# Kernel optimization log

Measured on AMD Instinct MI355X. Metric: run time of the kernel, lower is better.

The kernel has to match this reference:

```python
import jax, jax.numpy as jnp
import numpy as np

CN = 1024   # concept_num
H = 64      # hidden_dim
E = 64      # embedding_dim
RES_LEN = 2 # binary=True
B = 256     # batch (students)
D = H + E   # mlp_input_dim


def _mlp(x, W1, b1, W2, b2):
    # GKT MLP: relu(fc1) -> dropout(eval: identity) -> relu(fc2)
    return jax.nn.relu(jax.nn.relu(x @ W1 + b1) @ W2 + b2)


def setup_inputs() -> dict:
    key = jax.random.key(0)
    ks = jax.random.split(key, 20)
    s = 0.05
    nrm = lambda k, shape, scale=s: jax.random.normal(k, shape, dtype=jnp.float32) * scale
    zeros = lambda shape: jnp.zeros(shape, jnp.float32)
    return {
        "xt": jax.random.randint(ks[0], (B,), 0, RES_LEN * CN),
        "qt": jax.random.randint(ks[1], (B,), 0, CN),
        "ht": nrm(ks[2], (B, CN, H), 1.0),
        "graph": jax.random.uniform(ks[3], (CN, CN), dtype=jnp.float32),
        "emb_x": nrm(ks[4], (RES_LEN * CN, E), 1.0),
        "emb_c": nrm(ks[5], (CN + 1, E), 1.0).at[CN].set(0.0),  # padding row
        "fs_W1": nrm(ks[6], (D, H)), "fs_b1": zeros((H,)),
        "fs_W2": nrm(ks[7], (H, H)), "fs_b2": zeros((H,)),
        "fn0_W1": nrm(ks[8], (2 * D, H)), "fn0_b1": zeros((H,)),
        "fn0_W2": nrm(ks[9], (H, H)), "fn0_b2": zeros((H,)),
        "fn1_W1": nrm(ks[10], (2 * D, H)), "fn1_b1": zeros((H,)),
        "fn1_W2": nrm(ks[11], (H, H)), "fn1_b2": zeros((H,)),
        "ea_weight": jax.random.uniform(ks[12], (CN,), dtype=jnp.float32),
        "erase_W": nrm(ks[13], (H, H)), "erase_b": zeros((H,)),
        "add_W": nrm(ks[14], (H, H)), "add_b": zeros((H,)),
        "gru_Wih": nrm(ks[15], (H, 3 * H)), "gru_bih": zeros((3 * H,)),
        "gru_Whh": nrm(ks[16], (H, 3 * H)), "gru_bhh": zeros((3 * H,)),
        "pred_W": nrm(ks[17], (H, 1)), "pred_b": zeros((1,)),
    }


def _forward(xt, qt, graph, ht, emb_x, emb_c,
             fs_W1, fs_b1, fs_W2, fs_b2,
             fn0_W1, fn0_b1, fn0_W2, fn0_b2,
             fn1_W1, fn1_b1, fn1_W2, fn1_b2,
             ea_weight, erase_W, erase_b, add_W, add_b,
             gru_Wih, gru_bih, gru_Whh, gru_bhh, pred_W, pred_b):
    qt_mask = qt != -1                                   # [B]
    qts = jnp.clip(qt, 0, CN - 1)
    # ---------- _aggregate ----------
    res_emb = emb_x[xt]                                  # [B,E] == onehot(xt) @ emb_x
    base = jnp.where(qt_mask[:, None, None], emb_c[None, :CN, :], emb_c[CN][None, None, :])
    at_q = (jnp.arange(CN)[None, :] == qts[:, None]) & qt_mask[:, None]  # [B,CN]
    concept_emb = jnp.where(at_q[..., None], res_emb[:, None, :], base)  # [B,CN,E]
    tmp_ht = jnp.concatenate([ht, concept_emb], axis=-1)  # [B,CN,D]
    # ---------- _adj ----------
    adj = graph[qts][..., None]                          # [B,CN,1]
    radj = graph[:, qts].T[..., None]                    # [B,CN,1]
    # ---------- _agg_neighbors ----------
    self_ht = tmp_ht[jnp.arange(B), qts]                 # [B,D]
    self_feat = _mlp(self_ht, fs_W1, fs_b1, fs_W2, fs_b2)  # [B,H]
    neigh_ht = jnp.concatenate(
        [jnp.broadcast_to(self_ht[:, None, :], (B, CN, D)), tmp_ht], axis=-1)  # [B,CN,2D]
    neigh_feat = adj * _mlp(neigh_ht, fn0_W1, fn0_b1, fn0_W2, fn0_b2) \
               + radj * _mlp(neigh_ht, fn1_W1, fn1_b1, fn1_W2, fn1_b2)  # [B,CN,H]
    m_next = jnp.where(qt_mask[:, None, None], neigh_feat, ht)
    m_next = jnp.where(at_q[..., None], self_feat[:, None, :], m_next)
    # ---------- erase-add gate on masked rows ----------
    erase_g = jax.nn.sigmoid(m_next @ erase_W + erase_b)
    add_f = jnp.tanh(m_next @ add_W + add_b)
    w = ea_weight[None, :, None]                         # per-concept gate weight
    gated = m_next - w * erase_g * m_next + w * add_f
    m_next = jnp.where(qt_mask[:, None, None], gated, m_next)
    # ---------- GRUCell update on masked rows ----------
    gi = m_next @ gru_Wih + gru_bih                      # [B,CN,3H]
    gh = ht @ gru_Whh + gru_bhh
    i_r, i_z, i_n = jnp.split(gi, 3, axis=-1)
    h_r, h_z, h_n = jnp.split(gh, 3, axis=-1)
    r = jax.nn.sigmoid(i_r + h_r)
    z = jax.nn.sigmoid(i_z + h_z)
    n = jnp.tanh(i_n + r * h_n)
    h_gru = (1.0 - z) * n + z * ht
    h_next = jnp.where(qt_mask[:, None, None], h_gru, m_next)
    # ---------- _predict ----------
    y = (h_next @ pred_W + pred_b)[..., 0]               # [B,CN]
    y = jnp.where(qt_mask[:, None], jax.nn.sigmoid(y), y)
    return y


def reference(xt, qt, ht, graph, emb_x, emb_c,
              fs_W1, fs_b1, fs_W2, fs_b2,
              fn0_W1, fn0_b1, fn0_W2, fn0_b2,
              fn1_W1, fn1_b1, fn1_W2, fn1_b2,
              ea_weight, erase_W, erase_b, add_W, add_b,
              gru_Wih, gru_bih, gru_Whh, gru_bhh, pred_W, pred_b):
    return _forward(xt, qt, graph, ht, emb_x, emb_c,
                    fs_W1, fs_b1, fs_W2, fs_b2,
                    fn0_W1, fn0_b1, fn0_W2, fn0_b2,
                    fn1_W1, fn1_b1, fn1_W2, fn1_b2,
                    ea_weight, erase_W, erase_b, add_W, add_b,
                    gru_Wih, gru_bih, gru_Whh, gru_bhh, pred_W, pred_b)
```

## Files before the change

kernel.cpp:

```cpp
#include <hip/hip_runtime.h>
#include <hip/hip_bf16.h>

#define CN 1024
#define BN 256
#define SMEM_BYTES 155392

typedef __attribute__((ext_vector_type(4))) float f32x4;
typedef __attribute__((ext_vector_type(8))) short bf16x8;

__device__ __forceinline__ short f2bf(float f) {
    __hip_bfloat16 h = __float2bfloat16(f);
    return *reinterpret_cast<short*>(&h);
}
__device__ __forceinline__ float sigm(float x) {
    return __builtin_amdgcn_rcpf(1.f + __expf(-x));
}
__device__ __forceinline__ float tanh_fast(float x) {
    return 1.f - 2.f * __builtin_amdgcn_rcpf(1.f + __expf(2.f * x));
}

__global__ __launch_bounds__(256) void gkt_prep(
    const int* __restrict__ xt, const int* __restrict__ qt,
    const float* __restrict__ ht, const float* __restrict__ emb_x,
    const float* __restrict__ emb_c,
    const float* __restrict__ fs_W1, const float* __restrict__ fs_b1,
    const float* __restrict__ fs_W2, const float* __restrict__ fs_b2,
    const float* __restrict__ fn0_W1, const float* __restrict__ fn0_b1,
    const float* __restrict__ fn0_W2, const float* __restrict__ fn0_b2,
    const float* __restrict__ fn1_W1, const float* __restrict__ fn1_b1,
    const float* __restrict__ fn1_W2, const float* __restrict__ fn1_b2,
    const float* __restrict__ erase_W, const float* __restrict__ erase_b,
    const float* __restrict__ add_W, const float* __restrict__ add_b,
    const float* __restrict__ gru_Wih, const float* __restrict__ gru_bih,
    const float* __restrict__ gru_Whh, const float* __restrict__ gru_bhh,
    short* __restrict__ wrepack, float* __restrict__ biasc,
    float* __restrict__ perb, int* __restrict__ qtsA,
    int* __restrict__ maskA, int* __restrict__ xeA)
{
    int bid = blockIdx.x;
    int tid = threadIdx.x;
    int lane = tid & 63, wv = tid >> 6;
    __shared__ float inp[4][128];
    __shared__ float t1s[4][64];

    if (bid < 14) {
        int t = bid * 4 + wv;
        int colg = t * 16 + (lane & 15);
#pragma unroll
        for (int kh = 0; kh < 2; ++kh) {
            int k0 = kh * 32 + (lane >> 4) * 8;
            short v8[8];
#pragma unroll
            for (int j = 0; j < 8; ++j) {
                int k = k0 + j;
                float v;
                if (colg < 64)       v = fn0_W1[(128 + k) * 64 + colg];
                else if (colg < 128) v = fn1_W1[(128 + k) * 64 + (colg - 64)];
                else if (colg < 320) v = gru_Whh[k * 192 + (colg - 128)];
                else if (colg < 384) v = fn0_W2[k * 64 + (colg - 320)];
                else if (colg < 448) v = fn1_W2[k * 64 + (colg - 384)];
                else if (colg < 512) v = erase_W[k * 64 + (colg - 448)];
                else if (colg < 576) v = add_W[k * 64 + (colg - 512)];
                else if (colg < 768) v = gru_Wih[k * 192 + (colg - 576)];
                else if (colg < 832) v = fn0_W1[(192 + k) * 64 + (colg - 768)];
                else                 v = fn1_W1[(192 + k) * 64 + (colg - 832)];
                v8[j] = f2bf(v);
            }
            short* dst = wrepack + ((size_t)(t * 2 + kh) * 64 + lane) * 8;
#pragma unroll
            for (int j = 0; j < 8; ++j) dst[j] = v8[j];
        }
    } else if (bid == 14) {
        for (int g = tid; g < 768; g += 256) {
            float v;
            if (g < 64)       v = fn0_b1[g];
            else if (g < 128) v = fn1_b1[g - 64];
            else if (g < 320) v = gru_bhh[g - 128];
            else if (g < 384) v = fn0_b2[g - 320];
            else if (g < 448) v = fn1_b2[g - 384];
            else if (g < 512) v = erase_b[g - 448];
            else if (g < 576) v = add_b[g - 512];
            else              v = gru_bih[g - 576];
            biasc[g] = v;
        }
    } else {
        int b = (bid - 15) * 4 + wv;
        int qv = qt[b];
        int mki = (qv != -1);
        int qs = min(max(qv, 0), CN - 1);
        int xe = xt[b];
        float cq = mki ? emb_x[(size_t)xe * 64 + lane]
                       : emb_c[(size_t)CN * 64 + lane];
        inp[wv][lane]      = ht[((size_t)b * CN + qs) * 64 + lane];
        inp[wv][64 + lane] = cq;
        float p0 = 0.f, p1 = 0.f, fs = 0.f;
        for (int k = 0; k < 128; ++k) {
            float xk = inp[wv][k];
            p0 += xk * fn0_W1[k * 64 + lane];
            p1 += xk * fn1_W1[k * 64 + lane];
            fs += xk * fs_W1[k * 64 + lane];
        }
        t1s[wv][lane] = fmaxf(fs + fs_b1[lane], 0.f);
        float sf = 0.f;
        for (int k = 0; k < 64; ++k) sf += t1s[wv][k] * fs_W2[k * 64 + lane];
        sf = fmaxf(sf + fs_b2[lane], 0.f);
        float* pd = perb + (size_t)b * 192;
        pd[lane] = p0; pd[64 + lane] = p1; pd[128 + lane] = sf;
        if (lane == 0) { qtsA[b] = qs; maskA[b] = mki; xeA[b] = xe; }
    }
}

#define MFMA(a, bf, c) __builtin_amdgcn_mfma_f32_16x16x32_bf16((a), (bf), (c), 0, 0, 0)

__global__ __launch_bounds__(512, 1) void gkt_main(
    const float* __restrict__ ht, const float* __restrict__ graph,
    const float* __restrict__ ea_w, const float* __restrict__ pred_W,
    const float* __restrict__ pred_b,
    const short* __restrict__ wrepack, const float* __restrict__ biasc,
    const float* __restrict__ perb, const int* __restrict__ qtsA,
    const int* __restrict__ maskA, const int* __restrict__ xeA,
    const float* __restrict__ emb_x, const float* __restrict__ emb_c,
    float* __restrict__ out)
{
    extern __shared__ char smem[];
    short* FRs    = (short*)smem;
    float* s_bias = (float*)(smem + 114688);
    float* s_pre  = (float*)(smem + 117760);
    short* tiles  = (short*)(smem + 118528);

    int tid = threadIdx.x;
    int lane = tid & 63, w = tid >> 6;
    int l15 = lane & 15, q = lane >> 4;
    int b = blockIdx.x;

    short* s_x0 = tiles + w * 2304;
    short* s_x1 = s_x0 + 1152;

    {
        const f32x4* src = (const f32x4*)wrepack;
        f32x4* dst = (f32x4*)FRs;
        for (int i = tid; i < 7168; i += 512) dst[i] = src[i];
        for (int i = tid; i < 768; i += 512) s_bias[i] = biasc[i];
        const float* pd = perb + (size_t)b * 192;
        if (tid < 192) s_pre[tid] = pd[tid];
    }
    int qts = qtsA[b];
    int mk  = maskA[b];
    int xe  = xeA[b];
    __syncthreads();

    const bf16x8* FR = (const bf16x8*)FRs;
    f32x4 zero4 = {0.f, 0.f, 0.f, 0.f};
    float pb0 = pred_b[0];
    float pw[4];
#pragma unroll
    for (int t = 0; t < 4; ++t) pw[t] = pred_W[t * 16 + l15];

    for (int rt = 0; rt < 8; ++rt) {
        int c0 = w * 128 + rt * 16;
        const float* hrow = ht + ((size_t)b * CN + c0 + l15) * 64;
        f32x4 a0 = *(const f32x4*)(hrow + 8 * q);
        f32x4 a1 = *(const f32x4*)(hrow + 8 * q + 4);
        f32x4 a2 = *(const f32x4*)(hrow + 8 * q + 32);
        f32x4 a3 = *(const f32x4*)(hrow + 8 * q + 36);

        if (!mk) {
            f32x4 pwa = *(const f32x4*)(pred_W + 8 * q);
            f32x4 pwb = *(const f32x4*)(pred_W + 8 * q + 4);
            f32x4 pwc = *(const f32x4*)(pred_W + 8 * q + 32);
            f32x4 pwd = *(const f32x4*)(pred_W + 8 * q + 36);
            float part = 0.f;
#pragma unroll
            for (int i = 0; i < 4; ++i)
                part += a0[i] * pwa[i] + a1[i] * pwb[i] + a2[i] * pwc[i] + a3[i] * pwd[i];
            part += __shfl_xor(part, 16);
            part += __shfl_xor(part, 32);
            if (q == 0) out[(size_t)b * CN + c0 + l15] = part + pb0;
            continue;
        }

        int rq = c0 + l15;
        const float* ep = (rq == qts) ? (emb_x + (size_t)xe * 64)
                                      : (emb_c + (size_t)rq * 64);
        f32x4 e0 = *(const f32x4*)(ep + 8 * q);
        f32x4 e1 = *(const f32x4*)(ep + 8 * q + 4);
        f32x4 e2 = *(const f32x4*)(ep + 8 * q + 32);
        f32x4 e3 = *(const f32x4*)(ep + 8 * q + 36);

        bf16x8 hA0, hA1, cA0, cA1;
#pragma unroll
        for (int j = 0; j < 4; ++j) {
            hA0[j] = f2bf(a0[j]); hA0[4 + j] = f2bf(a1[j]);
            hA1[j] = f2bf(a2[j]); hA1[4 + j] = f2bf(a3[j]);
            cA0[j] = f2bf(e0[j]); cA0[4 + j] = f2bf(e1[j]);
            cA1[j] = f2bf(e2[j]); cA1[4 + j] = f2bf(e3[j]);
        }

        float adjv[4], radjv[4], eav[4];
#pragma unroll
        for (int r = 0; r < 4; ++r) {
            int cr = c0 + q * 4 + r;
            adjv[r]  = graph[(size_t)qts * CN + cr];
            radjv[r] = graph[(size_t)cr * CN + qts];
            eav[r]   = ea_w[cr];
        }
        float hv[4][4];
#pragma unroll
        for (int t = 0; t < 4; ++t)
#pragma unroll
            for (int r = 0; r < 4; ++r)
                hv[t][r] = ht[((size_t)b * CN + c0 + q * 4 + r) * 64 + t * 16 + l15];

#pragma unroll
        for (int t = 0; t < 8; ++t) {
            f32x4 acc = MFMA(hA0, FR[(2 * t) * 64 + lane], zero4);
            acc = MFMA(hA1, FR[(2 * t + 1) * 64 + lane], acc);
            acc = MFMA(cA0, FR[(96 + 2 * t) * 64 + lane], acc);
            acc = MFMA(cA1, FR[(97 + 2 * t) * 64 + lane], acc);
            int jl = (t & 3) * 16 + l15;
            float base = s_bias[t * 16 + l15] + ((t < 4) ? s_pre[jl] : s_pre[64 + jl]);
#pragma unroll
            for (int r = 0; r < 4; ++r) {
                float u = fmaxf(acc[r] + base, 0.f);
                if (t < 4) s_x0[(q * 4 + r) * 72 + jl] = f2bf(u);
                else       s_x1[(q * 4 + r) * 72 + jl] = f2bf(u);
            }
        }

        bf16x8 x0A0 = *(const bf16x8*)(s_x0 + l15 * 72 + 8 * q);
        bf16x8 x0A1 = *(const bf16x8*)(s_x0 + l15 * 72 + 32 + 8 * q);
        bf16x8 x1A0 = *(const bf16x8*)(s_x1 + l15 * 72 + 8 * q);
        bf16x8 x1A1 = *(const bf16x8*)(s_x1 + l15 * 72 + 32 + 8 * q);
        float mreg[4][4];
#pragma unroll
        for (int t = 0; t < 4; ++t) {
            f32x4 f0a = MFMA(x0A0, FR[(40 + 2 * t) * 64 + lane], zero4);
            f0a = MFMA(x0A1, FR[(41 + 2 * t) * 64 + lane], f0a);
            f32x4 f1a = MFMA(x1A0, FR[(48 + 2 * t) * 64 + lane], zero4);
            f1a = MFMA(x1A1, FR[(49 + 2 * t) * 64 + lane], f1a);
            int jl = t * 16 + l15;
            float b0 = s_bias[320 + jl], b1 = s_bias[384 + jl];
#pragma unroll
            for (int r = 0; r < 4; ++r) {
                int cr = c0 + q * 4 + r;
                float f0 = fmaxf(f0a[r] + b0, 0.f), f1 = fmaxf(f1a[r] + b1, 0.f);
                float mv = adjv[r] * f0 + radjv[r] * f1;
                if (cr == qts) mv = s_pre[128 + jl];
                mreg[t][r] = mv;
            }
        }
#pragma unroll
        for (int t = 0; t < 4; ++t)
#pragma unroll
            for (int r = 0; r < 4; ++r)
                s_x0[(q * 4 + r) * 72 + t * 16 + l15] = f2bf(mreg[t][r]);

        bf16x8 mA0 = *(const bf16x8*)(s_x0 + l15 * 72 + 8 * q);
        bf16x8 mA1 = *(const bf16x8*)(s_x0 + l15 * 72 + 32 + 8 * q);
#pragma unroll
        for (int t = 0; t < 4; ++t) {
            f32x4 eacc = MFMA(mA0, FR[(56 + 2 * t) * 64 + lane], zero4);
            eacc = MFMA(mA1, FR[(57 + 2 * t) * 64 + lane], eacc);
            f32x4 aacc = MFMA(mA0, FR[(64 + 2 * t) * 64 + lane], zero4);
            aacc = MFMA(mA1, FR[(65 + 2 * t) * 64 + lane], aacc);
            int jl = t * 16 + l15;
            float be = s_bias[448 + jl], ba = s_bias[512 + jl];
#pragma unroll
            for (int r = 0; r < 4; ++r) {
                float eg = sigm(eacc[r] + be);
                float af = tanh_fast(aacc[r] + ba);
                float mp = mreg[t][r] * (1.f - eav[r] * eg) + eav[r] * af;
                s_x1[(q * 4 + r) * 72 + jl] = f2bf(mp);
            }
        }

        bf16x8 mpA0 = *(const bf16x8*)(s_x1 + l15 * 72 + 8 * q);
        bf16x8 mpA1 = *(const bf16x8*)(s_x1 + l15 * 72 + 32 + 8 * q);
        float rg[4][4], ng[4][4];
#pragma unroll
        for (int t = 0; t < 4; ++t) {
            f32x4 gi = MFMA(mpA0, FR[(72 + 2 * t) * 64 + lane], zero4);
            gi = MFMA(mpA1, FR[(73 + 2 * t) * 64 + lane], gi);
            f32x4 gh = MFMA(hA0, FR[(16 + 2 * t) * 64 + lane], zero4);
            gh = MFMA(hA1, FR[(17 + 2 * t) * 64 + lane], gh);
            int jl = t * 16 + l15;
            float bi = s_bias[576 + jl], bh = s_bias[128 + jl];
#pragma unroll
            for (int r = 0; r < 4; ++r)
                rg[t][r] = sigm(gi[r] + bi + gh[r] + bh);
        }
#pragma unroll
        for (int t = 0; t < 4; ++t) {
            f32x4 gi = MFMA(mpA0, FR[(88 + 2 * t) * 64 + lane], zero4);
            gi = MFMA(mpA1, FR[(89 + 2 * t) * 64 + lane], gi);
            f32x4 gh = MFMA(hA0, FR[(32 + 2 * t) * 64 + lane], zero4);
            gh = MFMA(hA1, FR[(33 + 2 * t) * 64 + lane], gh);
            int jl = t * 16 + l15;
            float bi = s_bias[704 + jl], bh = s_bias[256 + jl];
#pragma unroll
            for (int r = 0; r < 4; ++r)
                ng[t][r] = tanh_fast(gi[r] + bi + rg[t][r] * (gh[r] + bh));
        }
        float yp[4] = {0.f, 0.f, 0.f, 0.f};
#pragma unroll
        for (int t = 0; t < 4; ++t) {
            f32x4 gi = MFMA(mpA0, FR[(80 + 2 * t) * 64 + lane], zero4);
            gi = MFMA(mpA1, FR[(81 + 2 * t) * 64 + lane], gi);
            f32x4 gh = MFMA(hA0, FR[(24 + 2 * t) * 64 + lane], zero4);
            gh = MFMA(hA1, FR[(25 + 2 * t) * 64 + lane], gh);
            int jl = t * 16 + l15;
            float bi = s_bias[640 + jl], bh = s_bias[192 + jl];
#pragma unroll
            for (int r = 0; r < 4; ++r) {
                float z = sigm(gi[r] + bi + gh[r] + bh);
                float hn = (1.f - z) * ng[t][r] + z * hv[t][r];
                yp[r] += hn * pw[t];
            }
        }
#pragma unroll
        for (int r = 0; r < 4; ++r) {
            float v = yp[r];
            v += __shfl_xor(v, 1);
            v += __shfl_xor(v, 2);
            v += __shfl_xor(v, 4);
            v += __shfl_xor(v, 8);
            if (l15 == 0) out[(size_t)b * CN + c0 + q * 4 + r] = sigm(v + pb0);
        }
    }
}

extern "C" void kernel_launch(void* const* d_in, const int* in_sizes, int n_in,
                              void* d_out, int out_size, void* d_ws, size_t ws_size,
                              hipStream_t stream) {
    (void)in_sizes; (void)n_in; (void)out_size; (void)ws_size;
    const int*   xt      = (const int*)d_in[0];
    const int*   qt      = (const int*)d_in[1];
    const float* ht      = (const float*)d_in[2];
    const float* graph   = (const float*)d_in[3];
    const float* emb_x   = (const float*)d_in[4];
    const float* emb_c   = (const float*)d_in[5];
    const float* fs_W1   = (const float*)d_in[6];
    const float* fs_b1   = (const float*)d_in[7];
    const float* fs_W2   = (const float*)d_in[8];
    const float* fs_b2   = (const float*)d_in[9];
    const float* fn0_W1  = (const float*)d_in[10];
    const float* fn0_b1  = (const float*)d_in[11];
    const float* fn0_W2  = (const float*)d_in[12];
    const float* fn0_b2  = (const float*)d_in[13];
    const float* fn1_W1  = (const float*)d_in[14];
    const float* fn1_b1  = (const float*)d_in[15];
    const float* fn1_W2  = (const float*)d_in[16];
    const float* fn1_b2  = (const float*)d_in[17];
    const float* ea_w    = (const float*)d_in[18];
    const float* erase_W = (const float*)d_in[19];
    const float* erase_b = (const float*)d_in[20];
    const float* add_W   = (const float*)d_in[21];
    const float* add_b   = (const float*)d_in[22];
    const float* gru_Wih = (const float*)d_in[23];
    const float* gru_bih = (const float*)d_in[24];
    const float* gru_Whh = (const float*)d_in[25];
    const float* gru_bhh = (const float*)d_in[26];
    const float* pred_W  = (const float*)d_in[27];
    const float* pred_b  = (const float*)d_in[28];

    char* ws = (char*)d_ws;
    short* wrepack = (short*)(ws);
    float* biasc   = (float*)(ws + 114688);
    float* perb    = (float*)(ws + 117760);
    int*   qtsA    = (int*)(ws + 314368);
    int*   maskA   = (int*)(ws + 315392);
    int*   xeA     = (int*)(ws + 316416);

    (void)hipFuncSetAttribute((const void*)gkt_main,
                              hipFuncAttributeMaxDynamicSharedMemorySize,
                              SMEM_BYTES);

    gkt_prep<<<79, 256, 0, stream>>>(
        xt, qt, ht, emb_x, emb_c,
        fs_W1, fs_b1, fs_W2, fs_b2,
        fn0_W1, fn0_b1, fn0_W2, fn0_b2,
        fn1_W1, fn1_b1, fn1_W2, fn1_b2,
        erase_W, erase_b, add_W, add_b,
        gru_Wih, gru_bih, gru_Whh, gru_bhh,
        wrepack, biasc, perb, qtsA, maskA, xeA);

    gkt_main<<<BN, 512, SMEM_BYTES, stream>>>(
        ht, graph, ea_w, pred_W, pred_b,
        wrepack, biasc, perb, qtsA, maskA, xeA,
        emb_x, emb_c, (float*)d_out);
}
```

Baseline: 219.8 us.

## Swap MFMA operand roles to keep activations in registers and drop LDS tiles

The MFMA operands are swapped so weights are the A operand and per-concept activations are the B operand, letting each layer's output feed the next layer straight from registers instead of round-tripping through per-wave LDS tiles. The weight repack permutes K order to match the register layout, and the r/z GRU biases are pre-summed. Block size doubles to 1024 threads with half the row tiles per wave, and LDS use shrinks. The risks are higher register pressure at 1024 threads and per-row scalar graph loads.

```diff
diff --git a/kernel.cpp b/kernel.cpp
--- a/kernel.cpp
+++ b/kernel.cpp
@@ -3,7 +3,7 @@
 
 #define CN 1024
 #define BN 256
-#define SMEM_BYTES 155392
+#define SMEM_BYTES 118016
 
 typedef __attribute__((ext_vector_type(4))) float f32x4;
 typedef __attribute__((ext_vector_type(8))) short bf16x8;
@@ -18,6 +18,7 @@
 __device__ __forceinline__ float tanh_fast(float x) {
     return 1.f - 2.f * __builtin_amdgcn_rcpf(1.f + __expf(2.f * x));
 }
+
 
 __global__ __launch_bounds__(256) void gkt_prep(
     const int* __restrict__ xt, const int* __restrict__ qt,
@@ -40,19 +41,19 @@
     int bid = blockIdx.x;
     int tid = threadIdx.x;
     int lane = tid & 63, wv = tid >> 6;
+    int l15 = lane & 15, q = lane >> 4;
     __shared__ float inp[4][128];
     __shared__ float t1s[4][64];
 
     if (bid < 14) {
         int t = bid * 4 + wv;
-        int colg = t * 16 + (lane & 15);
+        int colg = t * 16 + l15;
 #pragma unroll
         for (int kh = 0; kh < 2; ++kh) {
-            int k0 = kh * 32 + (lane >> 4) * 8;
             short v8[8];
 #pragma unroll
-            for (int j = 0; j < 8; ++j) {
-                int k = k0 + j;
+            for (int i = 0; i < 8; ++i) {
+                int k = kh * 32 + ((i >> 2) << 4) + (q << 2) + (i & 3);
                 float v;
                 if (colg < 64)       v = fn0_W1[(128 + k) * 64 + colg];
                 else if (colg < 128) v = fn1_W1[(128 + k) * 64 + (colg - 64)];
@@ -64,23 +65,25 @@
                 else if (colg < 768) v = gru_Wih[k * 192 + (colg - 576)];
                 else if (colg < 832) v = fn0_W1[(192 + k) * 64 + (colg - 768)];
                 else                 v = fn1_W1[(192 + k) * 64 + (colg - 832)];
-                v8[j] = f2bf(v);
+                v8[i] = f2bf(v);
             }
             short* dst = wrepack + ((size_t)(t * 2 + kh) * 64 + lane) * 8;
 #pragma unroll
-            for (int j = 0; j < 8; ++j) dst[j] = v8[j];
+            for (int i = 0; i < 8; ++i) dst[i] = v8[i];
         }
     } else if (bid == 14) {
-        for (int g = tid; g < 768; g += 256) {
+        for (int g = tid; g < 640; g += 256) {
             float v;
             if (g < 64)       v = fn0_b1[g];
             else if (g < 128) v = fn1_b1[g - 64];
-            else if (g < 320) v = gru_bhh[g - 128];
+            else if (g < 192) v = gru_bih[g - 128] + gru_bhh[g - 128];
+            else if (g < 256) v = gru_bih[g - 128] + gru_bhh[g - 128];
+            else if (g < 320) v = gru_bih[128 + (g - 256)];
             else if (g < 384) v = fn0_b2[g - 320];
             else if (g < 448) v = fn1_b2[g - 384];
             else if (g < 512) v = erase_b[g - 448];
             else if (g < 576) v = add_b[g - 512];
-            else              v = gru_bih[g - 576];
+            else              v = gru_bhh[128 + (g - 576)];
             biasc[g] = v;
         }
     } else {
@@ -110,9 +113,9 @@
     }
 }
 
-#define MFMA(a, bf, c) __builtin_amdgcn_mfma_f32_16x16x32_bf16((a), (bf), (c), 0, 0, 0)
-
-__global__ __launch_bounds__(512, 1) void gkt_main(
+#define MFMA(wa, xb, c) __builtin_amdgcn_mfma_f32_16x16x32_bf16((wa), (xb), (c), 0, 0, 0)
+
+__global__ __launch_bounds__(1024, 1) void gkt_main(
     const float* __restrict__ ht, const float* __restrict__ graph,
     const float* __restrict__ ea_w, const float* __restrict__ pred_W,
     const float* __restrict__ pred_b,
@@ -125,24 +128,20 @@
     extern __shared__ char smem[];
     short* FRs    = (short*)smem;
     float* s_bias = (float*)(smem + 114688);
-    float* s_pre  = (float*)(smem + 117760);
-    short* tiles  = (short*)(smem + 118528);
+    float* s_pre  = (float*)(smem + 117248);
 
     int tid = threadIdx.x;
     int lane = tid & 63, w = tid >> 6;
     int l15 = lane & 15, q = lane >> 4;
     int b = blockIdx.x;
 
-    short* s_x0 = tiles + w * 2304;
-    short* s_x1 = s_x0 + 1152;
-
     {
         const f32x4* src = (const f32x4*)wrepack;
         f32x4* dst = (f32x4*)FRs;
-        for (int i = tid; i < 7168; i += 512) dst[i] = src[i];
-        for (int i = tid; i < 768; i += 512) s_bias[i] = biasc[i];
+        for (int i = tid; i < 7168; i += 1024) dst[i] = src[i];
+        if (tid < 640) s_bias[tid] = biasc[tid];
         const float* pd = perb + (size_t)b * 192;
-        if (tid < 192) s_pre[tid] = pd[tid];
+        if (tid >= 640 && tid < 832) s_pre[tid - 640] = pd[tid - 640];
     }
     int qts = qtsA[b];
     int mk  = maskA[b];
@@ -152,180 +151,164 @@
     const bf16x8* FR = (const bf16x8*)FRs;
     f32x4 zero4 = {0.f, 0.f, 0.f, 0.f};
     float pb0 = pred_b[0];
-    float pw[4];
-#pragma unroll
-    for (int t = 0; t < 4; ++t) pw[t] = pred_W[t * 16 + l15];
-
-    for (int rt = 0; rt < 8; ++rt) {
-        int c0 = w * 128 + rt * 16;
-        const float* hrow = ht + ((size_t)b * CN + c0 + l15) * 64;
-        f32x4 a0 = *(const f32x4*)(hrow + 8 * q);
-        f32x4 a1 = *(const f32x4*)(hrow + 8 * q + 4);
-        f32x4 a2 = *(const f32x4*)(hrow + 8 * q + 32);
-        f32x4 a3 = *(const f32x4*)(hrow + 8 * q + 36);
+    f32x4 pw0 = *(const f32x4*)(pred_W + 4 * q);
+    f32x4 pw1 = *(const f32x4*)(pred_W + 16 + 4 * q);
+    f32x4 pw2 = *(const f32x4*)(pred_W + 32 + 4 * q);
+    f32x4 pw3 = *(const f32x4*)(pred_W + 48 + 4 * q);
+
+    for (int rt = 0; rt < 4; ++rt) {
+        int c0 = w * 64 + rt * 16;
+        int cr = c0 + l15;
+        const float* hrow = ht + ((size_t)b * CN + cr) * 64 + 4 * q;
+        f32x4 v0 = *(const f32x4*)(hrow);
+        f32x4 v1 = *(const f32x4*)(hrow + 16);
+        f32x4 v2 = *(const f32x4*)(hrow + 32);
+        f32x4 v3 = *(const f32x4*)(hrow + 48);
 
         if (!mk) {
-            f32x4 pwa = *(const f32x4*)(pred_W + 8 * q);
-            f32x4 pwb = *(const f32x4*)(pred_W + 8 * q + 4);
-            f32x4 pwc = *(const f32x4*)(pred_W + 8 * q + 32);
-            f32x4 pwd = *(const f32x4*)(pred_W + 8 * q + 36);
-            float part = 0.f;
+            float yp = 0.f;
 #pragma unroll
             for (int i = 0; i < 4; ++i)
-                part += a0[i] * pwa[i] + a1[i] * pwb[i] + a2[i] * pwc[i] + a3[i] * pwd[i];
-            part += __shfl_xor(part, 16);
-            part += __shfl_xor(part, 32);
-            if (q == 0) out[(size_t)b * CN + c0 + l15] = part + pb0;
+                yp += v0[i] * pw0[i] + v1[i] * pw1[i] + v2[i] * pw2[i] + v3[i] * pw3[i];
+            yp += __shfl_xor(yp, 16);
+            yp += __shfl_xor(yp, 32);
+            if (q == 0) out[(size_t)b * CN + cr] = yp + pb0;
             continue;
         }
 
-        int rq = c0 + l15;
-        const float* ep = (rq == qts) ? (emb_x + (size_t)xe * 64)
-                                      : (emb_c + (size_t)rq * 64);
-        f32x4 e0 = *(const f32x4*)(ep + 8 * q);
-        f32x4 e1 = *(const f32x4*)(ep + 8 * q + 4);
-        f32x4 e2 = *(const f32x4*)(ep + 8 * q + 32);
-        f32x4 e3 = *(const f32x4*)(ep + 8 * q + 36);
-
-        bf16x8 hA0, hA1, cA0, cA1;
-#pragma unroll
-        for (int j = 0; j < 4; ++j) {
-            hA0[j] = f2bf(a0[j]); hA0[4 + j] = f2bf(a1[j]);
-            hA1[j] = f2bf(a2[j]); hA1[4 + j] = f2bf(a3[j]);
-            cA0[j] = f2bf(e0[j]); cA0[4 + j] = f2bf(e1[j]);
-            cA1[j] = f2bf(e2[j]); cA1[4 + j] = f2bf(e3[j]);
-        }
-
-        float adjv[4], radjv[4], eav[4];
-#pragma unroll
-        for (int r = 0; r < 4; ++r) {
-            int cr = c0 + q * 4 + r;
-            adjv[r]  = graph[(size_t)qts * CN + cr];
-            radjv[r] = graph[(size_t)cr * CN + qts];
-            eav[r]   = ea_w[cr];
-        }
-        float hv[4][4];
-#pragma unroll
-        for (int t = 0; t < 4; ++t)
+        bool isq = (cr == qts);
+        const float* ep = isq ? (emb_x + (size_t)xe * 64)
+                              : (emb_c + (size_t)cr * 64);
+        f32x4 e0 = *(const f32x4*)(ep + 4 * q);
+        f32x4 e1 = *(const f32x4*)(ep + 16 + 4 * q);
+        f32x4 e2 = *(const f32x4*)(ep + 32 + 4 * q);
+        f32x4 e3 = *(const f32x4*)(ep + 48 + 4 * q);
+
+        bf16x8 hB0, hB1, cB0, cB1;
+#pragma unroll
+        for (int i = 0; i < 4; ++i) {
+            hB0[i] = f2bf(v0[i]); hB0[4 + i] = f2bf(v1[i]);
+            hB1[i] = f2bf(v2[i]); hB1[4 + i] = f2bf(v3[i]);
+            cB0[i] = f2bf(e0[i]); cB0[4 + i] = f2bf(e1[i]);
+            cB1[i] = f2bf(e2[i]); cB1[4 + i] = f2bf(e3[i]);
+        }
+
+        float adjs  = graph[(size_t)qts * CN + cr];
+        float radjs = graph[(size_t)cr * CN + qts];
+        float eas   = ea_w[cr];
+
+        bf16x8 x0B0, x0B1, x1B0, x1B1;
+#pragma unroll
+        for (int t = 0; t < 8; ++t) {
+            f32x4 acc = MFMA(FR[(2 * t) * 64 + lane], hB0, zero4);
+            acc = MFMA(FR[(2 * t + 1) * 64 + lane], hB1, acc);
+            acc = MFMA(FR[(96 + 2 * t) * 64 + lane], cB0, acc);
+            acc = MFMA(FR[(97 + 2 * t) * 64 + lane], cB1, acc);
+            int jb = (t & 3) * 16 + 4 * q;
+            f32x4 prev = *(const f32x4*)(s_pre + ((t < 4) ? 0 : 64) + jb);
+            f32x4 bv   = *(const f32x4*)(s_bias + t * 16 + 4 * q);
+#pragma unroll
+            for (int r = 0; r < 4; ++r) {
+                short us = f2bf(fmaxf(acc[r] + prev[r] + bv[r], 0.f));
+                if      (t == 0) x0B0[r] = us;
+                else if (t == 1) x0B0[4 + r] = us;
+                else if (t == 2) x0B1[r] = us;
+                else if (t == 3) x0B1[4 + r] = us;
+                else if (t == 4) x1B0[r] = us;
+                else if (t == 5) x1B0[4 + r] = us;
+                else if (t == 6) x1B1[r] = us;
+                else             x1B1[4 + r] = us;
+            }
+        }
+
+        f32x4 mreg0, mreg1, mreg2, mreg3;
+        bf16x8 mB0, mB1;
+#pragma unroll
+        for (int t = 0; t < 4; ++t) {
+            f32x4 f0a = MFMA(FR[(40 + 2 * t) * 64 + lane], x0B0, zero4);
+            f0a = MFMA(FR[(41 + 2 * t) * 64 + lane], x0B1, f0a);
+            f32x4 f1a = MFMA(FR[(48 + 2 * t) * 64 + lane], x1B0, zero4);
+            f1a = MFMA(FR[(49 + 2 * t) * 64 + lane], x1B1, f1a);
+            int jb = t * 16 + 4 * q;
+            f32x4 b0v = *(const f32x4*)(s_bias + 320 + jb);
+            f32x4 b1v = *(const f32x4*)(s_bias + 384 + jb);
+            f32x4 sfv = *(const f32x4*)(s_pre + 128 + jb);
+#pragma unroll
+            for (int r = 0; r < 4; ++r) {
+                float f0 = fmaxf(f0a[r] + b0v[r], 0.f);
+                float f1 = fmaxf(f1a[r] + b1v[r], 0.f);
+                float mv = adjs * f0 + radjs * f1;
+                mv = isq ? sfv[r] : mv;
+                if      (t == 0) { mreg0[r] = mv; mB0[r] = f2bf(mv); }
+                else if (t == 1) { mreg1[r] = mv; mB0[4 + r] = f2bf(mv); }
+                else if (t == 2) { mreg2[r] = mv; mB1[r] = f2bf(mv); }
+                else             { mreg3[r] = mv; mB1[4 + r] = f2bf(mv); }
+            }
+        }
+
+        bf16x8 pB0, pB1;
+#pragma unroll
+        for (int t = 0; t < 4; ++t) {
+            f32x4 eacc = MFMA(FR[(56 + 2 * t) * 64 + lane], mB0, zero4);
+            eacc = MFMA(FR[(57 + 2 * t) * 64 + lane], mB1, eacc);
+            f32x4 aacc = MFMA(FR[(64 + 2 * t) * 64 + lane], mB0, zero4);
+            aacc = MFMA(FR[(65 + 2 * t) * 64 + lane], mB1, aacc);
+            int jb = t * 16 + 4 * q;
+            f32x4 bev = *(const f32x4*)(s_bias + 448 + jb);
+            f32x4 bav = *(const f32x4*)(s_bias + 512 + jb);
+#pragma unroll
+            for (int r = 0; r < 4; ++r) {
+                float eg = sigm(eacc[r] + bev[r]);
+                float af = tanh_fast(aacc[r] + bav[r]);
+                float mr = (t == 0) ? mreg0[r] : (t == 1) ? mreg1[r]
+                         : (t == 2) ? mreg2[r] : mreg3[r];
+                float mp = mr * (1.f - eas * eg) + eas * af;
+                if      (t == 0) pB0[r] = f2bf(mp);
+                else if (t == 1) pB0[4 + r] = f2bf(mp);
+                else if (t == 2) pB1[r] = f2bf(mp);
+                else             pB1[4 + r] = f2bf(mp);
+            }
+        }
+
+        float yp = 0.f;
+#pragma unroll
+        for (int t = 0; t < 4; ++t) {
+            int jb = t * 16 + 4 * q;
+            f32x4 gir = MFMA(FR[(72 + 2 * t) * 64 + lane], pB0, zero4);
+            gir = MFMA(FR[(73 + 2 * t) * 64 + lane], pB1, gir);
+            f32x4 ghr = MFMA(FR[(16 + 2 * t) * 64 + lane], hB0, zero4);
+            ghr = MFMA(FR[(17 + 2 * t) * 64 + lane], hB1, ghr);
+            f32x4 brv = *(const f32x4*)(s_bias + 128 + jb);
+            f32x4 rg;
+#pragma unroll
+            for (int r = 0; r < 4; ++r) rg[r] = sigm(gir[r] + ghr[r] + brv[r]);
+            f32x4 gin = MFMA(FR[(88 + 2 * t) * 64 + lane], pB0, zero4);
+            gin = MFMA(FR[(89 + 2 * t) * 64 + lane], pB1, gin);
+            f32x4 ghn = MFMA(FR[(32 + 2 * t) * 64 + lane], hB0, zero4);
+            ghn = MFMA(FR[(33 + 2 * t) * 64 + lane], hB1, ghn);
+            f32x4 binv = *(const f32x4*)(s_bias + 256 + jb);
+            f32x4 bhnv = *(const f32x4*)(s_bias + 576 + jb);
+            f32x4 ng;
 #pragma unroll
             for (int r = 0; r < 4; ++r)
-                hv[t][r] = ht[((size_t)b * CN + c0 + q * 4 + r) * 64 + t * 16 + l15];
-
-#pragma unroll
-        for (int t = 0; t < 8; ++t) {
-            f32x4 acc = MFMA(hA0, FR[(2 * t) * 64 + lane], zero4);
-            acc = MFMA(hA1, FR[(2 * t + 1) * 64 + lane], acc);
-            acc = MFMA(cA0, FR[(96 + 2 * t) * 64 + lane], acc);
-            acc = MFMA(cA1, FR[(97 + 2 * t) * 64 + lane], acc);
-            int jl = (t & 3) * 16 + l15;
-            float base = s_bias[t * 16 + l15] + ((t < 4) ? s_pre[jl] : s_pre[64 + jl]);
+                ng[r] = tanh_fast(gin[r] + binv[r] + rg[r] * (ghn[r] + bhnv[r]));
+            f32x4 giz = MFMA(FR[(80 + 2 * t) * 64 + lane], pB0, zero4);
+            giz = MFMA(FR[(81 + 2 * t) * 64 + lane], pB1, giz);
+            f32x4 ghz = MFMA(FR[(24 + 2 * t) * 64 + lane], hB0, zero4);
+            ghz = MFMA(FR[(25 + 2 * t) * 64 + lane], hB1, ghz);
+            f32x4 bzv = *(const f32x4*)(s_bias + 192 + jb);
+            f32x4 hvv = (t == 0) ? v0 : (t == 1) ? v1 : (t == 2) ? v2 : v3;
+            f32x4 pwv = (t == 0) ? pw0 : (t == 1) ? pw1 : (t == 2) ? pw2 : pw3;
 #pragma unroll
             for (int r = 0; r < 4; ++r) {
-                float u = fmaxf(acc[r] + base, 0.f);
-                if (t < 4) s_x0[(q * 4 + r) * 72 + jl] = f2bf(u);
-                else       s_x1[(q * 4 + r) * 72 + jl] = f2bf(u);
-            }
-        }
-
-        bf16x8 x0A0 = *(const bf16x8*)(s_x0 + l15 * 72 + 8 * q);
-        bf16x8 x0A1 = *(const bf16x8*)(s_x0 + l15 * 72 + 32 + 8 * q);
-        bf16x8 x1A0 = *(const bf16x8*)(s_x1 + l15 * 72 + 8 * q);
-        bf16x8 x1A1 = *(const bf16x8*)(s_x1 + l15 * 72 + 32 + 8 * q);
-        float mreg[4][4];
-#pragma unroll
-        for (int t = 0; t < 4; ++t) {
-            f32x4 f0a = MFMA(x0A0, FR[(40 + 2 * t) * 64 + lane], zero4);
-            f0a = MFMA(x0A1, FR[(41 + 2 * t) * 64 + lane], f0a);
-            f32x4 f1a = MFMA(x1A0, FR[(48 + 2 * t) * 64 + lane], zero4);
-            f1a = MFMA(x1A1, FR[(49 + 2 * t) * 64 + lane], f1a);
-            int jl = t * 16 + l15;
-            float b0 = s_bias[320 + jl], b1 = s_bias[384 + jl];
-#pragma unroll
-            for (int r = 0; r < 4; ++r) {
-                int cr = c0 + q * 4 + r;
-                float f0 = fmaxf(f0a[r] + b0, 0.f), f1 = fmaxf(f1a[r] + b1, 0.f);
-                float mv = adjv[r] * f0 + radjv[r] * f1;
-                if (cr == qts) mv = s_pre[128 + jl];
-                mreg[t][r] = mv;
-            }
-        }
-#pragma unroll
-        for (int t = 0; t < 4; ++t)
-#pragma unroll
-            for (int r = 0; r < 4; ++r)
-                s_x0[(q * 4 + r) * 72 + t * 16 + l15] = f2bf(mreg[t][r]);
-
-        bf16x8 mA0 = *(const bf16x8*)(s_x0 + l15 * 72 + 8 * q);
-        bf16x8 mA1 = *(const bf16x8*)(s_x0 + l15 * 72 + 32 + 8 * q);
-#pragma unroll
-        for (int t = 0; t < 4; ++t) {
-            f32x4 eacc = MFMA(mA0, FR[(56 + 2 * t) * 64 + lane], zero4);
-            eacc = MFMA(mA1, FR[(57 + 2 * t) * 64 + lane], eacc);
-            f32x4 aacc = MFMA(mA0, FR[(64 + 2 * t) * 64 + lane], zero4);
-            aacc = MFMA(mA1, FR[(65 + 2 * t) * 64 + lane], aacc);
-            int jl = t * 16 + l15;
-            float be = s_bias[448 + jl], ba = s_bias[512 + jl];
-#pragma unroll
-            for (int r = 0; r < 4; ++r) {
-                float eg = sigm(eacc[r] + be);
-                float af = tanh_fast(aacc[r] + ba);
-                float mp = mreg[t][r] * (1.f - eav[r] * eg) + eav[r] * af;
-                s_x1[(q * 4 + r) * 72 + jl] = f2bf(mp);
-            }
-        }
-
-        bf16x8 mpA0 = *(const bf16x8*)(s_x1 + l15 * 72 + 8 * q);
-        bf16x8 mpA1 = *(const bf16x8*)(s_x1 + l15 * 72 + 32 + 8 * q);
-        float rg[4][4], ng[4][4];
-#pragma unroll
-        for (int t = 0; t < 4; ++t) {
-            f32x4 gi = MFMA(mpA0, FR[(72 + 2 * t) * 64 + lane], zero4);
-            gi = MFMA(mpA1, FR[(73 + 2 * t) * 64 + lane], gi);
-            f32x4 gh = MFMA(hA0, FR[(16 + 2 * t) * 64 + lane], zero4);
-            gh = MFMA(hA1, FR[(17 + 2 * t) * 64 + lane], gh);
-            int jl = t * 16 + l15;
-            float bi = s_bias[576 + jl], bh = s_bias[128 + jl];
-#pragma unroll
-            for (int r = 0; r < 4; ++r)
-                rg[t][r] = sigm(gi[r] + bi + gh[r] + bh);
-        }
-#pragma unroll
-        for (int t = 0; t < 4; ++t) {
-            f32x4 gi = MFMA(mpA0, FR[(88 + 2 * t) * 64 + lane], zero4);
-            gi = MFMA(mpA1, FR[(89 + 2 * t) * 64 + lane], gi);
-            f32x4 gh = MFMA(hA0, FR[(32 + 2 * t) * 64 + lane], zero4);
-            gh = MFMA(hA1, FR[(33 + 2 * t) * 64 + lane], gh);
-            int jl = t * 16 + l15;
-            float bi = s_bias[704 + jl], bh = s_bias[256 + jl];
-#pragma unroll
-            for (int r = 0; r < 4; ++r)
-                ng[t][r] = tanh_fast(gi[r] + bi + rg[t][r] * (gh[r] + bh));
-        }
-        float yp[4] = {0.f, 0.f, 0.f, 0.f};
-#pragma unroll
-        for (int t = 0; t < 4; ++t) {
-            f32x4 gi = MFMA(mpA0, FR[(80 + 2 * t) * 64 + lane], zero4);
-            gi = MFMA(mpA1, FR[(81 + 2 * t) * 64 + lane], gi);
-            f32x4 gh = MFMA(hA0, FR[(24 + 2 * t) * 64 + lane], zero4);
-            gh = MFMA(hA1, FR[(25 + 2 * t) * 64 + lane], gh);
-            int jl = t * 16 + l15;
-            float bi = s_bias[640 + jl], bh = s_bias[192 + jl];
-#pragma unroll
-            for (int r = 0; r < 4; ++r) {
-                float z = sigm(gi[r] + bi + gh[r] + bh);
-                float hn = (1.f - z) * ng[t][r] + z * hv[t][r];
-                yp[r] += hn * pw[t];
-            }
-        }
-#pragma unroll
-        for (int r = 0; r < 4; ++r) {
-            float v = yp[r];
-            v += __shfl_xor(v, 1);
-            v += __shfl_xor(v, 2);
-            v += __shfl_xor(v, 4);
-            v += __shfl_xor(v, 8);
-            if (l15 == 0) out[(size_t)b * CN + c0 + q * 4 + r] = sigm(v + pb0);
-        }
+                float z = sigm(giz[r] + ghz[r] + bzv[r]);
+                float hn = (1.f - z) * ng[r] + z * hvv[r];
+                yp += hn * pwv[r];
+            }
+        }
+        yp += __shfl_xor(yp, 16);
+        yp += __shfl_xor(yp, 32);
+        if (q == 0) out[(size_t)b * CN + cr] = sigm(yp + pb0);
     }
 }
 
@@ -384,7 +367,7 @@
         gru_Wih, gru_bih, gru_Whh, gru_bhh,
         wrepack, biasc, perb, qtsA, maskA, xeA);
 
-    gkt_main<<<BN, 512, SMEM_BYTES, stream>>>(
+    gkt_main<<<BN, 1024, SMEM_BYTES, stream>>>(
         ht, graph, ea_w, pred_W, pred_b,
         wrepack, biasc, perb, qtsA, maskA, xeA,
         emb_x, emb_c, (float*)d_out);
```

After: 277.9 us. 26.4% more time.
